# Kernel optimization log

Measured on AMD Instinct MI355X. Metric: run time of the kernel, lower is better.

## Reference

```python
import jax, jax.numpy as jnp
import numpy as np
import math

B, T = 8, 1024
IN_DIMS = 1024
OUT_DIMS = 1024
NUM_CODES = 1024
NUM_CODEBOOKS = 8


def setup_inputs() -> dict:
    key = jax.random.key(0)
    k1, k2, k3, k4, k5 = jax.random.split(key, 5)
    x = jax.random.normal(k1, (B, T, IN_DIMS), dtype=jnp.float32)
    target = jax.random.randint(k2, (B, T, NUM_CODEBOOKS), 0, NUM_CODES, dtype=jnp.int64)
    # params, init per reset_params()
    codebook = jax.random.normal(k3, (NUM_CODES, NUM_CODEBOOKS, OUT_DIMS), dtype=jnp.float32) / math.sqrt(OUT_DIMS * NUM_CODEBOOKS)
    proj_w = jax.random.normal(k4, (NUM_CODEBOOKS * NUM_CODES, IN_DIMS), dtype=jnp.float32) / math.sqrt(IN_DIMS)
    proj_b = jnp.zeros((NUM_CODEBOOKS * NUM_CODES,), dtype=jnp.float32)
    wproj_w = jax.random.normal(k5, (NUM_CODEBOOKS, IN_DIMS), dtype=jnp.float32) / math.sqrt(IN_DIMS)
    return {"x": x, "target": target, "codebook": codebook,
            "proj_w": proj_w, "proj_b": proj_b, "wproj_w": wproj_w}


def reference(x, target, codebook, proj_w, proj_b, wproj_w):
    # xp: (B, T, K, C)
    xp = (jnp.einsum('btd,nd->btn', x, proj_w) + proj_b).reshape(B, T, NUM_CODEBOOKS, NUM_CODES)
    # xw: (B, T, K) softmax codebook weights
    xw = jax.nn.softmax(jnp.einsum('btd,kd->btk', x, wproj_w), axis=-1)
    # gather codebook embeddings under no_grad: codebook[target, arange(K)] -> (B, T, K, D)
    cb_inds = jnp.arange(NUM_CODEBOOKS)
    codebook_embs = jax.lax.stop_gradient(codebook[target, cb_inds])
    # per-element cross entropy, reduction='none' -> (B, T, K)
    logp = jax.nn.log_softmax(xp, axis=-1)
    x_loss = -jnp.take_along_axis(logp, target[..., None], axis=-1)[..., 0]
    # softmax-weighted sum over codebooks -> (B, T, D)
    emb = jnp.einsum('btkd,btk->btd', codebook_embs, xw)
    return emb, x_loss
```

## Files before the change

kernel.cpp:

```cpp
#include <hip/hip_runtime.h>
#include <hip/hip_bf16.h>
#include <math.h>

#define MTOT   8192
#define KDIM   1024
#define NCODES 1024
#define NCB    8
#define NTOT   (NCODES*NCB)
#define ODIM   1024

#define BM 128
#define BN 128
#define BK 32
#define NTILES (NTOT/BN)

typedef __attribute__((ext_vector_type(8))) short  bf16x8;
typedef __attribute__((ext_vector_type(4))) float  f32x4;

__device__ __forceinline__ ushort f2bf(float f) {
  union { float f; unsigned u; } v; v.f = f;
  unsigned u = v.u;
  unsigned r = (u + 0x7fffu + ((u >> 16) & 1u)) >> 16;
  return (ushort)r;
}

__device__ __forceinline__ void gload16(const void* g, void* l) {
  __builtin_amdgcn_global_load_lds(
      (const __attribute__((address_space(1))) void*)g,
      (__attribute__((address_space(3))) void*)l,
      16, 0, 0);
}

__global__ void cvt_bf16_kernel(const float* __restrict__ in,
                                ushort* __restrict__ out) {
  int i = blockIdx.x * blockDim.x + threadIdx.x;
  float4 v = ((const float4*)in)[i];
  ushort4 o;
  o.x = f2bf(v.x); o.y = f2bf(v.y); o.z = f2bf(v.z); o.w = f2bf(v.w);
  ((ushort4*)out)[i] = o;
}

__global__ void ce_gemm_kernel(const ushort* __restrict__ Abf,
                               const ushort* __restrict__ Bbf,
                               const float*  __restrict__ bias,
                               const int*    __restrict__ target,
                               float* __restrict__ partials,
                               float* __restrict__ tgtlogit) {
  __shared__ ushort As[BM * BK];
  __shared__ ushort Bs[BN * BK];
  __shared__ float  redM[2][BM];
  __shared__ float  redS[2][BM];

  const int tid   = threadIdx.x;
  const int wid   = tid >> 6;
  const int lane  = tid & 63;
  const int mtile = blockIdx.x;
  const int ntile = blockIdx.y;
  const int wr    = wid >> 1;
  const int wc    = wid & 1;
  const int g     = lane >> 4;
  const int c15   = lane & 15;

  f32x4 acc[4][4];
#pragma unroll
  for (int m = 0; m < 4; ++m)
#pragma unroll
    for (int n = 0; n < 4; ++n)
      acc[m][n] = (f32x4){0.f, 0.f, 0.f, 0.f};

  const ushort* gA0 = Abf + (size_t)(mtile * BM + (tid >> 2)) * KDIM + (tid & 3) * 8;
  const ushort* gB0 = Bbf + (size_t)(ntile * BN + (tid >> 2)) * KDIM + (tid & 3) * 8;
  ushort* lA = As + wid * 64 * 8;
  ushort* lB = Bs + wid * 64 * 8;

  for (int kt = 0; kt < KDIM / BK; ++kt) {
    const ushort* ga = gA0 + kt * BK;
    const ushort* gb = gB0 + kt * BK;
    gload16(ga,               lA);
    gload16(ga + 64 * KDIM,   lA + 2048);
    gload16(gb,               lB);
    gload16(gb + 64 * KDIM,   lB + 2048);
    __syncthreads();

    bf16x8 af[4], bfr[4];
#pragma unroll
    for (int m = 0; m < 4; ++m)
      af[m] = *(const bf16x8*)&As[(wr * 64 + m * 16 + c15) * BK + g * 8];
#pragma unroll
    for (int n = 0; n < 4; ++n)
      bfr[n] = *(const bf16x8*)&Bs[(wc * 64 + n * 16 + c15) * BK + g * 8];
#pragma unroll
    for (int m = 0; m < 4; ++m)
#pragma unroll
      for (int n = 0; n < 4; ++n)
        acc[m][n] = __builtin_amdgcn_mfma_f32_16x16x32_bf16(af[m], bfr[n], acc[m][n], 0, 0, 0);
    __syncthreads();
  }

  const int kcb = ntile >> 3;
  float bias_n[4];
#pragma unroll
  for (int n = 0; n < 4; ++n)
    bias_n[n] = bias[ntile * 128 + wc * 64 + n * 16 + c15];

  float rmax[4][4];
#pragma unroll
  for (int m = 0; m < 4; ++m)
#pragma unroll
    for (int j = 0; j < 4; ++j) {
      float v = acc[m][0][j] + bias_n[0];
      v = fmaxf(v, acc[m][1][j] + bias_n[1]);
      v = fmaxf(v, acc[m][2][j] + bias_n[2]);
      v = fmaxf(v, acc[m][3][j] + bias_n[3]);
#pragma unroll
      for (int off = 1; off < 16; off <<= 1)
        v = fmaxf(v, __shfl_xor(v, off));
      rmax[m][j] = v;
    }

  const int col_base = ntile * 128 + wc * 64;
  float rsum[4][4];
#pragma unroll
  for (int m = 0; m < 4; ++m) {
    const int rowg = mtile * 128 + wr * 64 + m * 16 + g * 4;
#pragma unroll
    for (int j = 0; j < 4; ++j) {
      const int row  = rowg + j;
      const int t    = target[row * NCB + kcb];
      const int tcol = kcb * NCODES + t;
      float s = 0.f;
#pragma unroll
      for (int n = 0; n < 4; ++n) {
        const float v = acc[m][n][j] + bias_n[n];
        const int col = col_base + n * 16 + c15;
        if (col == tcol) tgtlogit[row * NCB + kcb] = v;
        s += __expf(v - rmax[m][j]);
      }
#pragma unroll
      for (int off = 1; off < 16; off <<= 1)
        s += __shfl_xor(s, off);
      rsum[m][j] = s;
    }
  }

  if (c15 == 0) {
#pragma unroll
    for (int m = 0; m < 4; ++m)
#pragma unroll
      for (int j = 0; j < 4; ++j) {
        const int rl = wr * 64 + m * 16 + g * 4 + j;
        redM[wc][rl] = rmax[m][j];
        redS[wc][rl] = rsum[m][j];
      }
  }
  __syncthreads();
  if (tid < BM) {
    const float m0 = redM[0][tid], m1 = redM[1][tid];
    const float s0 = redS[0][tid], s1 = redS[1][tid];
    const float Mx = fmaxf(m0, m1);
    const float S  = s0 * __expf(m0 - Mx) + s1 * __expf(m1 - Mx);
    const int row  = mtile * 128 + tid;
    partials[((size_t)row * NTILES + ntile) * 2 + 0] = Mx;
    partials[((size_t)row * NTILES + ntile) * 2 + 1] = S;
  }
}

__global__ void lse_reduce_kernel(const float* __restrict__ partials,
                                  const float* __restrict__ tgtlogit,
                                  float* __restrict__ xloss_out) {
  const int idx = blockIdx.x * blockDim.x + threadIdx.x;
  if (idx >= MTOT * NCB) return;
  const int row = idx >> 3, k = idx & 7;
  float M = -1e30f, S = 0.f;
#pragma unroll
  for (int i = 0; i < 8; ++i) {
    const int nt = k * 8 + i;
    const float m = partials[((size_t)row * NTILES + nt) * 2 + 0];
    const float s = partials[((size_t)row * NTILES + nt) * 2 + 1];
    const float Mn = fmaxf(M, m);
    S = S * __expf(M - Mn) + s * __expf(m - Mn);
    M = Mn;
  }
  xloss_out[idx] = M + __logf(S) - tgtlogit[idx];
}

__global__ void emb_kernel(const float* __restrict__ x,
                           const int*   __restrict__ target,
                           const float* __restrict__ cb,
                           const float* __restrict__ wproj,
                           float* __restrict__ emb_out) {
  const int bt   = blockIdx.x;
  const int tid  = threadIdx.x;
  const int lane = tid & 63;
  const int wid  = tid >> 6;

  const float4 xv = ((const float4*)(x + (size_t)bt * KDIM))[tid];
  float p[8];
#pragma unroll
  for (int k = 0; k < 8; ++k) {
    const float4 wv = ((const float4*)(wproj + k * KDIM))[tid];
    p[k] = xv.x * wv.x + xv.y * wv.y + xv.z * wv.z + xv.w * wv.w;
  }
#pragma unroll
  for (int k = 0; k < 8; ++k)
#pragma unroll
    for (int off = 32; off >= 1; off >>= 1)
      p[k] += __shfl_xor(p[k], off);

  __shared__ float lred[4][8];
  if (lane == 0) {
#pragma unroll
    for (int k = 0; k < 8; ++k) lred[wid][k] = p[k];
  }
  __syncthreads();

  float logit[8], mx = -1e30f;
#pragma unroll
  for (int k = 0; k < 8; ++k) {
    logit[k] = lred[0][k] + lred[1][k] + lred[2][k] + lred[3][k];
    mx = fmaxf(mx, logit[k]);
  }
  float w[8], den = 0.f;
#pragma unroll
  for (int k = 0; k < 8; ++k) { w[k] = __expf(logit[k] - mx); den += w[k]; }
  const float inv = 1.f / den;

  float4 a = make_float4(0.f, 0.f, 0.f, 0.f);
#pragma unroll
  for (int k = 0; k < 8; ++k) {
    const int t = target[bt * NCB + k];
    const float4 cv = ((const float4*)(cb + ((size_t)t * NCB + k) * ODIM))[tid];
    const float wk = w[k] * inv;
    a.x += wk * cv.x; a.y += wk * cv.y; a.z += wk * cv.z; a.w += wk * cv.w;
  }
  ((float4*)(emb_out + (size_t)bt * ODIM))[tid] = a;
}

extern "C" void kernel_launch(void* const* d_in, const int* in_sizes, int n_in,
                              void* d_out, int out_size, void* d_ws, size_t ws_size,
                              hipStream_t stream) {
  const float* x        = (const float*)d_in[0];
  const int*   target   = (const int*)  d_in[1];
  const float* codebook = (const float*)d_in[2];
  const float* proj_w   = (const float*)d_in[3];
  const float* proj_b   = (const float*)d_in[4];
  const float* wproj_w  = (const float*)d_in[5];

  float* out       = (float*)d_out;
  float* emb_out   = out;
  float* xloss_out = out + (size_t)MTOT * ODIM;

  char* ws = (char*)d_ws;
  ushort* xbf      = (ushort*)ws;
  ushort* wbf      = (ushort*)(ws + (size_t)16 * 1024 * 1024);
  float*  partials = (float*) (ws + (size_t)32 * 1024 * 1024);
  float*  tgtlogit = (float*) (ws + (size_t)36 * 1024 * 1024);

  cvt_bf16_kernel<<<(MTOT * KDIM / 4) / 256, 256, 0, stream>>>(x,      xbf);
  cvt_bf16_kernel<<<(NTOT * KDIM / 4) / 256, 256, 0, stream>>>(proj_w, wbf);

  dim3 grid(MTOT / BM, NTOT / BN);
  ce_gemm_kernel<<<grid, 256, 0, stream>>>(xbf, wbf, proj_b, target, partials, tgtlogit);

  lse_reduce_kernel<<<(MTOT * NCB) / 256, 256, 0, stream>>>(partials, tgtlogit, xloss_out);

  emb_kernel<<<MTOT, 256, 0, stream>>>(x, target, codebook, wproj_w, emb_out);
}
```

Before: 228.3 us.

## Rewrite CE GEMM as 256x256 tiled, double-buffered, swizzled-LDS pipelined kernel

Replaces the 128x128 single-buffered GEMM with a 256x256 block tile using 8 waves and 128 KB of dynamic LDS. A double-buffered 64-wide K stage uses a swizzled layout, and async global-to-LDS loads are interleaved with MFMA phases under explicit barriers, waitcnts and setprio. The aim is to cut global traffic per FLOP, hide load latency and avoid LDS bank conflicts. Partials shrink to 32 N-tiles per row, so the LSE reduction loop is shortened to match. Risks are lower occupancy and one block per CU from the large LDS use, plus fragile hand scheduling.

```diff
diff --git a/kernel.cpp b/kernel.cpp
--- a/kernel.cpp
+++ b/kernel.cpp
@@ -6,13 +6,12 @@
 #define KDIM   1024
 #define NCODES 1024
 #define NCB    8
-#define NTOT   (NCODES*NCB)
+#define NTOT   8192
 #define ODIM   1024
 
-#define BM 128
-#define BN 128
-#define BK 32
-#define NTILES (NTOT/BN)
+#define BM 256
+#define BN 256
+#define NTILES_N 32
 
 typedef __attribute__((ext_vector_type(8))) short  bf16x8;
 typedef __attribute__((ext_vector_type(4))) float  f32x4;
@@ -40,72 +39,161 @@
   ((ushort4*)out)[i] = o;
 }
 
-__global__ void ce_gemm_kernel(const ushort* __restrict__ Abf,
-                               const ushort* __restrict__ Bbf,
-                               const float*  __restrict__ bias,
-                               const int*    __restrict__ target,
-                               float* __restrict__ partials,
-                               float* __restrict__ tgtlogit) {
-  __shared__ ushort As[BM * BK];
-  __shared__ ushort Bs[BN * BK];
-  __shared__ float  redM[2][BM];
-  __shared__ float  redS[2][BM];
-
-  const int tid   = threadIdx.x;
-  const int wid   = tid >> 6;
-  const int lane  = tid & 63;
+
+__device__ __forceinline__ void chunk_dec(int c, int& srcA, int& srcB) {
+  const int q  = c >> 6;
+  const int sq = q >> 1;
+  const int ct = q & 1;
+  const int r4 = (c >> 2) & 15;
+  const int cb = (((c & 3) ^ ((c >> 3) & 3)) << 4);
+  const int rtA = (sq & 3) + ((sq >> 2) << 3);
+  const int rtB = (sq & 1) + ((sq >> 1) << 2);
+  srcA = ((rtA << 4) + r4) * (KDIM * 2) + ct * 64 + cb;
+  srcB = ((rtB << 4) + r4) * (KDIM * 2) + ct * 64 + cb;
+}
+
+#define STAGE_A(T, H) do { \
+    gload16(Ag + (size_t)(srcA0 + (H)*131072 + (T)*128), ldsA_st + ((T)&1)*32768 + (H)*16384); \
+    gload16(Ag + (size_t)(srcA1 + (H)*131072 + (T)*128), ldsA_st + ((T)&1)*32768 + (H)*16384 + 8192); \
+  } while(0)
+#define STAGE_B(T, H) do { \
+    gload16(Bg + (size_t)(srcB0 + (H)*65536 + (T)*128), ldsB_st + ((T)&1)*32768 + (H)*16384); \
+    gload16(Bg + (size_t)(srcB1 + (H)*65536 + (T)*128), ldsB_st + ((T)&1)*32768 + (H)*16384 + 8192); \
+  } while(0)
+
+#define LDA_Q(P, MH) do { \
+    _Pragma("unroll") for (int m_ = 0; m_ < 4; ++m_) \
+    _Pragma("unroll") for (int k_ = 0; k_ < 2; ++k_) \
+      a[m_][k_] = *(const bf16x8*)(ldsA_rd + (P)*32768 + (MH)*16384 + m_*2048 + k_*1024); \
+  } while(0)
+#define LDB_Q(P, NH, B) do { \
+    _Pragma("unroll") for (int n_ = 0; n_ < 2; ++n_) \
+    _Pragma("unroll") for (int k_ = 0; k_ < 2; ++k_) \
+      B[n_][k_] = *(const bf16x8*)(ldsB_rd + (P)*32768 + (NH)*16384 + n_*2048 + k_*1024); \
+  } while(0)
+#define MM_Q(MH, NH, B) do { \
+    _Pragma("unroll") for (int m_ = 0; m_ < 4; ++m_) \
+    _Pragma("unroll") for (int n_ = 0; n_ < 2; ++n_) \
+    _Pragma("unroll") for (int k_ = 0; k_ < 2; ++k_) \
+      acc[(MH)*4+m_][(NH)*2+n_] = __builtin_amdgcn_mfma_f32_16x16x32_bf16( \
+          a[m_][k_], B[n_][k_], acc[(MH)*4+m_][(NH)*2+n_], 0, 0, 0); \
+  } while(0)
+
+#define PH_MID(MH, NH, B) \
+    __builtin_amdgcn_s_barrier(); \
+    asm volatile("s_waitcnt lgkmcnt(0)" ::: "memory"); \
+    __builtin_amdgcn_sched_barrier(0); \
+    __builtin_amdgcn_s_setprio(1); \
+    MM_Q(MH, NH, B); \
+    __builtin_amdgcn_s_setprio(0);
+#define PH_END \
+    __builtin_amdgcn_s_barrier(); \
+    asm volatile("" ::: "memory");
+
+__global__ __launch_bounds__(512)
+void ce_gemm_kernel(const ushort* __restrict__ Abf,
+                    const ushort* __restrict__ Bbf,
+                    const float*  __restrict__ bias,
+                    const int*    __restrict__ target,
+                    float* __restrict__ partials,
+                    float* __restrict__ tgtlogit) {
+  extern __shared__ char smem[];
+
+  const int tid  = threadIdx.x;
+  const int wid  = tid >> 6;
+  const int lane = tid & 63;
+  const int wr   = wid >> 2;
+  const int wc   = wid & 3;
+  const int g    = lane >> 4;
+  const int c15  = lane & 15;
   const int mtile = blockIdx.x;
   const int ntile = blockIdx.y;
-  const int wr    = wid >> 1;
-  const int wc    = wid & 1;
-  const int g     = lane >> 4;
-  const int c15   = lane & 15;
-
-  f32x4 acc[4][4];
-#pragma unroll
-  for (int m = 0; m < 4; ++m)
+
+  const int swz = (c15 * 64 + g * 16) ^ ((c15 & 6) << 3);
+  const char* ldsA_rd = smem + wr * 8192 + swz;
+  const char* ldsB_rd = smem + 65536 + wc * 4096 + swz;
+  char* ldsA_st = smem + wid * 1024;
+  char* ldsB_st = smem + 65536 + wid * 1024;
+
+  const char* Ag = ((const char*)Abf) + (size_t)mtile * 256 * (KDIM * 2);
+  const char* Bg = ((const char*)Bbf) + (size_t)ntile * 256 * (KDIM * 2);
+  int srcA0, srcB0, srcA1, srcB1;
+  chunk_dec(tid,       srcA0, srcB0);
+  chunk_dec(tid + 512, srcA1, srcB1);
+
+  f32x4 acc[8][4];
+#pragma unroll
+  for (int m = 0; m < 8; ++m)
 #pragma unroll
     for (int n = 0; n < 4; ++n)
       acc[m][n] = (f32x4){0.f, 0.f, 0.f, 0.f};
 
-  const ushort* gA0 = Abf + (size_t)(mtile * BM + (tid >> 2)) * KDIM + (tid & 3) * 8;
-  const ushort* gB0 = Bbf + (size_t)(ntile * BN + (tid >> 2)) * KDIM + (tid & 3) * 8;
-  ushort* lA = As + wid * 64 * 8;
-  ushort* lB = Bs + wid * 64 * 8;
-
-  for (int kt = 0; kt < KDIM / BK; ++kt) {
-    const ushort* ga = gA0 + kt * BK;
-    const ushort* gb = gB0 + kt * BK;
-    gload16(ga,               lA);
-    gload16(ga + 64 * KDIM,   lA + 2048);
-    gload16(gb,               lB);
-    gload16(gb + 64 * KDIM,   lB + 2048);
-    __syncthreads();
-
-    bf16x8 af[4], bfr[4];
-#pragma unroll
-    for (int m = 0; m < 4; ++m)
-      af[m] = *(const bf16x8*)&As[(wr * 64 + m * 16 + c15) * BK + g * 8];
-#pragma unroll
-    for (int n = 0; n < 4; ++n)
-      bfr[n] = *(const bf16x8*)&Bs[(wc * 64 + n * 16 + c15) * BK + g * 8];
-#pragma unroll
-    for (int m = 0; m < 4; ++m)
-#pragma unroll
-      for (int n = 0; n < 4; ++n)
-        acc[m][n] = __builtin_amdgcn_mfma_f32_16x16x32_bf16(af[m], bfr[n], acc[m][n], 0, 0, 0);
-    __syncthreads();
-  }
-
-  const int kcb = ntile >> 3;
+  bf16x8 a[4][2], b0[2][2], b1[2][2];
+
+  STAGE_A(0, 0); STAGE_A(0, 1); STAGE_B(0, 0); STAGE_B(0, 1);
+  STAGE_A(1, 0); STAGE_B(1, 1);
+  asm volatile("s_waitcnt vmcnt(4)" ::: "memory");
+  __builtin_amdgcn_s_barrier();
+  asm volatile("" ::: "memory");
+
+#pragma unroll 1
+  for (int i = 0; i < 7; ++i) {
+    const int t1 = 2 * i + 1;
+    LDA_Q(0, 0); LDB_Q(0, 0, b0);
+    STAGE_A(t1, 1);
+    PH_MID(0, 0, b0) PH_END
+    LDB_Q(0, 1, b1);
+    STAGE_B(t1, 0);
+    PH_MID(0, 1, b1) PH_END
+    LDA_Q(0, 1);
+    STAGE_A(t1 + 1, 0);
+    PH_MID(1, 1, b1) PH_END
+    STAGE_B(t1 + 1, 1);
+    PH_MID(1, 0, b0)
+    asm volatile("s_waitcnt vmcnt(4)" ::: "memory");
+    PH_END
+    LDA_Q(1, 0); LDB_Q(1, 0, b0);
+    STAGE_A(t1 + 1, 1);
+    PH_MID(0, 0, b0) PH_END
+    LDB_Q(1, 1, b1);
+    STAGE_B(t1 + 1, 0);
+    PH_MID(0, 1, b1) PH_END
+    LDA_Q(1, 1);
+    STAGE_A(t1 + 2, 0);
+    PH_MID(1, 1, b1) PH_END
+    STAGE_B(t1 + 2, 1);
+    PH_MID(1, 0, b0)
+    asm volatile("s_waitcnt vmcnt(4)" ::: "memory");
+    PH_END
+  }
+  LDA_Q(0, 0); LDB_Q(0, 0, b0);
+  STAGE_A(15, 1);
+  PH_MID(0, 0, b0) PH_END
+  LDB_Q(0, 1, b1);
+  STAGE_B(15, 0);
+  PH_MID(0, 1, b1) PH_END
+  LDA_Q(0, 1);
+  PH_MID(1, 1, b1) PH_END
+  PH_MID(1, 0, b0)
+  asm volatile("s_waitcnt vmcnt(0)" ::: "memory");
+  PH_END
+  LDA_Q(1, 0); LDB_Q(1, 0, b0);
+  PH_MID(0, 0, b0) PH_END
+  LDB_Q(1, 1, b1);
+  PH_MID(0, 1, b1) PH_END
+  LDA_Q(1, 1);
+  PH_MID(1, 1, b1) PH_END
+  PH_MID(1, 0, b0) PH_END
+
+  const int kcb = ntile >> 2;
   float bias_n[4];
 #pragma unroll
   for (int n = 0; n < 4; ++n)
-    bias_n[n] = bias[ntile * 128 + wc * 64 + n * 16 + c15];
-
-  float rmax[4][4];
-#pragma unroll
-  for (int m = 0; m < 4; ++m)
+    bias_n[n] = bias[ntile * 256 + wc * 64 + n * 16 + c15];
+
+  float rmax[8][4], rsum[8][4];
+#pragma unroll
+  for (int m = 0; m < 8; ++m)
 #pragma unroll
     for (int j = 0; j < 4; ++j) {
       float v = acc[m][0][j] + bias_n[0];
@@ -118,11 +206,10 @@
       rmax[m][j] = v;
     }
 
-  const int col_base = ntile * 128 + wc * 64;
-  float rsum[4][4];
-#pragma unroll
-  for (int m = 0; m < 4; ++m) {
-    const int rowg = mtile * 128 + wr * 64 + m * 16 + g * 4;
+  const int col_base = ntile * 256 + wc * 64;
+#pragma unroll
+  for (int m = 0; m < 8; ++m) {
+    const int rowg = mtile * 256 + wr * 128 + m * 16 + g * 4;
 #pragma unroll
     for (int j = 0; j < 4; ++j) {
       const int row  = rowg + j;
@@ -132,8 +219,7 @@
 #pragma unroll
       for (int n = 0; n < 4; ++n) {
         const float v = acc[m][n][j] + bias_n[n];
-        const int col = col_base + n * 16 + c15;
-        if (col == tcol) tgtlogit[row * NCB + kcb] = v;
+        if (col_base + n * 16 + c15 == tcol) tgtlogit[row * NCB + kcb] = v;
         s += __expf(v - rmax[m][j]);
       }
 #pragma unroll
@@ -143,25 +229,33 @@
     }
   }
 
+  __syncthreads();
+  float* redM = (float*)smem;
+  float* redS = redM + 1024;
   if (c15 == 0) {
 #pragma unroll
-    for (int m = 0; m < 4; ++m)
+    for (int m = 0; m < 8; ++m)
 #pragma unroll
       for (int j = 0; j < 4; ++j) {
-        const int rl = wr * 64 + m * 16 + g * 4 + j;
-        redM[wc][rl] = rmax[m][j];
-        redS[wc][rl] = rsum[m][j];
+        const int rl = wr * 128 + m * 16 + g * 4 + j;
+        redM[wc * 256 + rl] = rmax[m][j];
+        redS[wc * 256 + rl] = rsum[m][j];
       }
   }
   __syncthreads();
-  if (tid < BM) {
-    const float m0 = redM[0][tid], m1 = redM[1][tid];
-    const float s0 = redS[0][tid], s1 = redS[1][tid];
-    const float Mx = fmaxf(m0, m1);
-    const float S  = s0 * __expf(m0 - Mx) + s1 * __expf(m1 - Mx);
-    const int row  = mtile * 128 + tid;
-    partials[((size_t)row * NTILES + ntile) * 2 + 0] = Mx;
-    partials[((size_t)row * NTILES + ntile) * 2 + 1] = S;
+  if (tid < 256) {
+    float M = redM[tid], S = redS[tid];
+#pragma unroll
+    for (int w = 1; w < 4; ++w) {
+      const float m2 = redM[w * 256 + tid];
+      const float s2 = redS[w * 256 + tid];
+      const float Mx = fmaxf(M, m2);
+      S = S * __expf(M - Mx) + s2 * __expf(m2 - Mx);
+      M = Mx;
+    }
+    const int row = mtile * 256 + tid;
+    partials[((size_t)row * NTILES_N + ntile) * 2 + 0] = M;
+    partials[((size_t)row * NTILES_N + ntile) * 2 + 1] = S;
   }
 }
 
@@ -173,10 +267,10 @@
   const int row = idx >> 3, k = idx & 7;
   float M = -1e30f, S = 0.f;
 #pragma unroll
-  for (int i = 0; i < 8; ++i) {
-    const int nt = k * 8 + i;
-    const float m = partials[((size_t)row * NTILES + nt) * 2 + 0];
-    const float s = partials[((size_t)row * NTILES + nt) * 2 + 1];
+  for (int i = 0; i < 4; ++i) {
+    const int nt = k * 4 + i;
+    const float m = partials[((size_t)row * NTILES_N + nt) * 2 + 0];
+    const float s = partials[((size_t)row * NTILES_N + nt) * 2 + 1];
     const float Mn = fmaxf(M, m);
     S = S * __expf(M - Mn) + s * __expf(m - Mn);
     M = Mn;
@@ -225,15 +319,15 @@
   for (int k = 0; k < 8; ++k) { w[k] = __expf(logit[k] - mx); den += w[k]; }
   const float inv = 1.f / den;
 
-  float4 a = make_float4(0.f, 0.f, 0.f, 0.f);
+  float4 acc = make_float4(0.f, 0.f, 0.f, 0.f);
 #pragma unroll
   for (int k = 0; k < 8; ++k) {
     const int t = target[bt * NCB + k];
     const float4 cv = ((const float4*)(cb + ((size_t)t * NCB + k) * ODIM))[tid];
     const float wk = w[k] * inv;
-    a.x += wk * cv.x; a.y += wk * cv.y; a.z += wk * cv.z; a.w += wk * cv.w;
-  }
-  ((float4*)(emb_out + (size_t)bt * ODIM))[tid] = a;
+    acc.x += wk * cv.x; acc.y += wk * cv.y; acc.z += wk * cv.z; acc.w += wk * cv.w;
+  }
+  ((float4*)(emb_out + (size_t)bt * ODIM))[tid] = acc;
 }
 
 extern "C" void kernel_launch(void* const* d_in, const int* in_sizes, int n_in,
@@ -254,13 +348,17 @@
   ushort* xbf      = (ushort*)ws;
   ushort* wbf      = (ushort*)(ws + (size_t)16 * 1024 * 1024);
   float*  partials = (float*) (ws + (size_t)32 * 1024 * 1024);
-  float*  tgtlogit = (float*) (ws + (size_t)36 * 1024 * 1024);
+  float*  tgtlogit = (float*) (ws + (size_t)35 * 1024 * 1024);
+
+  hipFuncSetAttribute((const void*)ce_gemm_kernel,
+                      hipFuncAttributeMaxDynamicSharedMemorySize, 131072);
 
   cvt_bf16_kernel<<<(MTOT * KDIM / 4) / 256, 256, 0, stream>>>(x,      xbf);
   cvt_bf16_kernel<<<(NTOT * KDIM / 4) / 256, 256, 0, stream>>>(proj_w, wbf);
 
   dim3 grid(MTOT / BM, NTOT / BN);
-  ce_gemm_kernel<<<grid, 256, 0, stream>>>(xbf, wbf, proj_b, target, partials, tgtlogit);
+  ce_gemm_kernel<<<grid, 512, 131072, stream>>>(xbf, wbf, proj_b, target,
+                                                partials, tgtlogit);
 
   lse_reduce_kernel<<<(MTOT * NCB) / 256, 256, 0, stream>>>(partials, tgtlogit, xloss_out);
 
```

Result: faster. 208.6 us (-8.6%).
